# Kernel tuning notes

Measured on AMD Instinct MI355X. Metric: run time of the kernel, lower is better.

Reference implementation:

```python
import jax, jax.numpy as jnp
import numpy as np

NS = (50000, 12500, 3125, 800, 200)   # mesh vertex counts per hierarchy level
CS = (3, 16, 32, 64, 128)             # in_channels + out_channels per level
S = 9       # spiral length
K = 4       # nnz per row of pooling transforms
LATENT = 128
B = 32


def setup_inputs() -> dict:
    key = jax.random.key(0)
    ks = iter(jax.random.split(key, 80))
    inp = {"x": jax.random.normal(next(ks), (B, NS[0], 3), jnp.float32)}
    for l in range(4):
        inp["spiral%d" % l] = jax.random.randint(next(ks), (NS[l], S), 0, NS[l], dtype=jnp.int32)
        # down_transform[l]: sparse (NS[l+1], NS[l])
        inp["down_rows%d" % l] = jnp.repeat(jnp.arange(NS[l + 1], dtype=jnp.int32), K)
        inp["down_cols%d" % l] = jax.random.randint(next(ks), (NS[l + 1] * K,), 0, NS[l], dtype=jnp.int32)
        inp["down_vals%d" % l] = jnp.full((NS[l + 1] * K,), 1.0 / K, jnp.float32)
        # up_transform[l]: sparse (NS[l], NS[l+1])
        inp["up_rows%d" % l] = jnp.repeat(jnp.arange(NS[l], dtype=jnp.int32), K)
        inp["up_cols%d" % l] = jax.random.randint(next(ks), (NS[l] * K,), 0, NS[l + 1], dtype=jnp.int32)
        inp["up_vals%d" % l] = jnp.full((NS[l] * K,), 1.0 / K, jnp.float32)
        # encoder SpiralConv weights: Linear(C_in*S -> C_out), stored (in, out)
        inp["enW%d" % l] = jax.random.normal(next(ks), (CS[l] * S, CS[l + 1]), jnp.float32) * 0.05
        inp["enb%d" % l] = jnp.zeros((CS[l + 1],), jnp.float32)
    inp["muW"] = jax.random.normal(next(ks), (NS[4] * CS[4], LATENT), jnp.float32) * 0.02
    inp["mub"] = jnp.zeros((LATENT,), jnp.float32)
    inp["deW0"] = jax.random.normal(next(ks), (LATENT, NS[4] * CS[4]), jnp.float32) * 0.02
    inp["deb0"] = jnp.zeros((NS[4] * CS[4],), jnp.float32)
    dcin = (CS[4], CS[4], CS[3], CS[2])
    dcout = (CS[4], CS[3], CS[2], CS[1])
    for i in range(4):
        inp["dW%d" % i] = jax.random.normal(next(ks), (dcin[i] * S, dcout[i]), jnp.float32) * 0.05
        inp["db%d" % i] = jnp.zeros((dcout[i],), jnp.float32)
    inp["outW"] = jax.random.normal(next(ks), (CS[1] * S, 3), jnp.float32) * 0.05
    inp["outb"] = jnp.zeros((3,), jnp.float32)
    return inp


def _sconv(x, idx, W, b):
    # x: (B, N, C); idx: (N, S) -> gather spiral neighbors, flatten, dense Linear
    g = x[:, idx.reshape(-1), :].reshape(x.shape[0], idx.shape[0], -1)  # (B, N, S*C)
    return g @ W + b


def _pool(x, rows, cols, vals, M):
    # sparse (M, N) transform applied along vertex dim: index_select + scale + scatter_add
    out = jnp.zeros((x.shape[0], M, x.shape[2]), x.dtype)
    return out.at[:, rows].add(x[:, cols] * vals[None, :, None])


def _forward(x, spirals, downs, ups, enWs, enbs, muW, mub, deW0, deb0, dWs, dbs, outW, outb):
    # encode: (SpiralConv -> ELU -> Pool) x4
    h = x
    for l in range(4):
        h = jax.nn.elu(_sconv(h, spirals[l], enWs[l], enbs[l]))
        h = _pool(h, downs[l][0], downs[l][1], downs[l][2], NS[l + 1])
    h = h.reshape(h.shape[0], -1)  # (B, num_vert * C_last)
    mu = jax.nn.sigmoid(h @ muW + mub)  # is_vae=False path: sigmoid(mu), logvar=None
    z = mu
    # decode: Linear -> (Pool -> SpiralConv -> ELU) x4 -> SpiralConv
    d = (z @ deW0 + deb0).reshape(-1, NS[4], CS[4])
    for i in range(4):
        l = 3 - i
        d = _pool(d, ups[l][0], ups[l][1], ups[l][2], NS[l])
        d = jax.nn.elu(_sconv(d, spirals[l], dWs[i], dbs[i]))
    out = _sconv(d, spirals[0], outW, outb)
    return out, z, mu


def reference(x, spiral0, down_rows0, down_cols0, down_vals0, up_rows0, up_cols0, up_vals0, enW0, enb0, spiral1, down_rows1, down_cols1, down_vals1, up_rows1, up_cols1, up_vals1, enW1, enb1, spiral2, down_rows2, down_cols2, down_vals2, up_rows2, up_cols2, up_vals2, enW2, enb2, spiral3, down_rows3, down_cols3, down_vals3, up_rows3, up_cols3, up_vals3, enW3, enb3, muW, mub, deW0, deb0, dW0, db0, dW1, db1, dW2, db2, dW3, db3, outW, outb):
    spirals = [spiral0, spiral1, spiral2, spiral3]
    downs = [(down_rows0, down_cols0, down_vals0), (down_rows1, down_cols1, down_vals1), (down_rows2, down_cols2, down_vals2), (down_rows3, down_cols3, down_vals3)]
    ups = [(up_rows0, up_cols0, up_vals0), (up_rows1, up_cols1, up_vals1), (up_rows2, up_cols2, up_vals2), (up_rows3, up_cols3, up_vals3)]
    return _forward(x, spirals, downs, ups, [enW0, enW1, enW2, enW3], [enb0, enb1, enb2, enb3], muW, mub, deW0, deb0, [dW0, dW1, dW2, dW3], [db0, db1, db2, db3], outW, outb)
```

## Files before the change

### kernel.cpp

```cpp
#include <hip/hip_runtime.h>
#include <hip/hip_bf16.h>
#include <math.h>

#define NS0 50000
#define NS1 12500
#define NS2 3125
#define NS3 800
#define NS4 200
#define BATCH 32
#define SLEN 9

typedef __hip_bfloat16 bf16;
typedef __attribute__((ext_vector_type(8))) short short8_t;
typedef __attribute__((ext_vector_type(4))) float f32x4;

struct WcvAll {
    const float* W[9];
    bf16* dst[9];
    int K[9], CO[9], KP[9];
    int off[10];
};

__global__ void __launch_bounds__(256)
wconv_all_kernel(WcvAll p)
{
    int gid = blockIdx.x * 256 + threadIdx.x;
    if (gid >= p.off[9]) return;
    int seg = 0;
    #pragma unroll
    for (int s = 1; s < 9; ++s) seg += (gid >= p.off[s]);
    int local = gid - p.off[seg];
    int NKK = p.KP[seg] >> 5;
    int jj   = local & 7;
    int g8   = local >> 3;
    int lane = g8 & 63;
    int blk  = g8 >> 6;
    int kk   = blk % NKK;
    int cb   = blk / NKK;
    int col0 = lane & 15, kh = lane >> 4;
    int co = cb * 16 + col0;
    int k  = kk * 32 + kh * 8 + jj;
    float v = (k < p.K[seg] && co < p.CO[seg]) ? p.W[seg][k * p.CO[seg] + co] : 0.f;
    p.dst[seg][local] = __float2bfloat16(v);
}

__global__ void __launch_bounds__(256)
xpose_in_kernel(const float* __restrict__ x, bf16* __restrict__ xT)
{
    int tid = blockIdx.x * 256 + threadIdx.x;
    if (tid >= BATCH * NS0) return;
    int b = tid / NS0, n = tid - b * NS0;
    const float* src = x + (size_t)tid * 3;
    bf16* dst = xT + ((size_t)n * 32 + b) * 3;
    dst[0] = __float2bfloat16(src[0]);
    dst[1] = __float2bfloat16(src[1]);
    dst[2] = __float2bfloat16(src[2]);
}

__global__ void __launch_bounds__(256)
xpose_out_kernel(const float* __restrict__ vm, float* __restrict__ out)
{
    int tid = blockIdx.x * 256 + threadIdx.x;
    if (tid >= BATCH * NS0) return;
    int b = tid / NS0, n = tid - b * NS0;
    const float* src = vm + ((size_t)n * 32 + b) * 3;
    float* dst = out + (size_t)tid * 3;
    dst[0] = src[0];
    dst[1] = src[1];
    dst[2] = src[2];
}

__global__ void __launch_bounds__(256)
sconv_enc0(const bf16* __restrict__ xT, const int* __restrict__ idx,
           const bf16* __restrict__ Wfrag, const float* __restrict__ bias,
           bf16* __restrict__ y)
{
    __shared__ short lds[64 * 40];
    const int t = threadIdx.x;
    const int n0 = blockIdx.x * 2;

    for (int e = t; e < 64 * 5; e += 256) {
        int r = e / 5, k = 27 + (e - r * 5);
        lds[r * 40 + k] = 0;
    }
    for (int e = t; e < 2 * 9 * 32; e += 256) {
        int v = e / 288;
        int rem = e - v * 288;
        int s = rem >> 5, b = rem & 31;
        int j = idx[(n0 + v) * 9 + s];
        const short* src = (const short*)(xT + (size_t)j * 96 + b * 3);
        short* dst = &lds[(v * 32 + b) * 40 + s * 3];
        dst[0] = src[0];
        dst[1] = src[1];
        dst[2] = src[2];
    }
    __syncthreads();

    const int w = t >> 6, lane = t & 63;
    const int col0 = lane & 15, kh = lane >> 4;
    const int rbase = w * 16;
    float bv = bias[col0];
    f32x4 acc = (f32x4){bv, bv, bv, bv};
    short8_t bfr = *(const short8_t*)(Wfrag + (size_t)lane * 8);
    short8_t afr = *(const short8_t*)&lds[(rbase + col0) * 40 + kh * 8];
    acc = __builtin_amdgcn_mfma_f32_16x16x32_bf16(afr, bfr, acc, 0, 0, 0);
    #pragma unroll
    for (int i = 0; i < 4; ++i) {
        int rl = rbase + kh * 4 + i;
        float v = acc[i];
        v = v > 0.f ? v : expm1f(v);
        y[((size_t)n0 * 32 + rl) * 16 + col0] = __float2bfloat16(v);
    }
}

template<int CIN, int COUT, int COP, int ACT, int NN, typename TOUT>
__global__ void __launch_bounds__(256)
sconv_vm(const bf16* __restrict__ x, const int* __restrict__ idx,
         const bf16* __restrict__ Wfrag, const float* __restrict__ bias,
         TOUT* __restrict__ y)
{
    constexpr int KP  = (9 * CIN + 31) / 32 * 32;
    constexpr int NKK = KP / 32;
    constexpr int NCB = COP / 16;

    const int t = threadIdx.x, w = t >> 6, lane = t & 63;
    const int n = blockIdx.x * 4 + w;
    if (n >= NN) return;
    const int col0 = lane & 15, kh = lane >> 4;

    int jn[9];
    #pragma unroll
    for (int s = 0; s < 9; ++s) jn[s] = idx[n * 9 + s];

    f32x4 acc[2][NCB];
    #pragma unroll
    for (int cb = 0; cb < NCB; ++cb) {
        int col = cb * 16 + col0;
        float bv = (col < COUT) ? bias[col] : 0.f;
        acc[0][cb] = (f32x4){bv, bv, bv, bv};
        acc[1][cb] = (f32x4){bv, bv, bv, bv};
    }

    const short8_t z8 = {0, 0, 0, 0, 0, 0, 0, 0};
    #pragma unroll
    for (int kk = 0; kk < NKK; ++kk) {
        short8_t a0 = z8, a1 = z8;
        if constexpr (CIN == 16) {
            const int hi = kh >> 1;
            const int ch = (kh & 1) * 8;
            if (kk < 4) {
                int j = hi ? jn[2 * kk + 1] : jn[2 * kk];
                const bf16* base = x + (size_t)j * 512 + ch;
                a0 = *(const short8_t*)(base + col0 * 16);
                a1 = *(const short8_t*)(base + 256 + col0 * 16);
            } else {
                if (!hi) {
                    int j = jn[8];
                    const bf16* base = x + (size_t)j * 512 + ch;
                    a0 = *(const short8_t*)(base + col0 * 16);
                    a1 = *(const short8_t*)(base + 256 + col0 * 16);
                }
            }
        } else {
            constexpr int SPK = CIN / 32;
            const int j = jn[kk / SPK];
            const int ch = (kk % SPK) * 32 + kh * 8;
            const bf16* base = x + (size_t)j * (32 * CIN) + ch;
            a0 = *(const short8_t*)(base + col0 * CIN);
            a1 = *(const short8_t*)(base + (16 + col0) * CIN);
        }
        #pragma unroll
        for (int cb = 0; cb < NCB; ++cb) {
            short8_t bfr = *(const short8_t*)(Wfrag + ((size_t)(cb * NKK + kk) * 64 + lane) * 8);
            acc[0][cb] = __builtin_amdgcn_mfma_f32_16x16x32_bf16(a0, bfr, acc[0][cb], 0, 0, 0);
            acc[1][cb] = __builtin_amdgcn_mfma_f32_16x16x32_bf16(a1, bfr, acc[1][cb], 0, 0, 0);
        }
    }

    #pragma unroll
    for (int f = 0; f < 2; ++f) {
        #pragma unroll
        for (int cb = 0; cb < NCB; ++cb) {
            int col = cb * 16 + col0;
            if (col < COUT) {
                #pragma unroll
                for (int i = 0; i < 4; ++i) {
                    int b = f * 16 + kh * 4 + i;
                    float v = acc[f][cb][i];
                    if (ACT) v = v > 0.f ? v : expm1f(v);
                    TOUT* dst = &y[((size_t)n * 32 + b) * COUT + col];
                    if constexpr (__is_same(TOUT, float)) *dst = v;
                    else *dst = __float2bfloat16(v);
                }
            }
        }
    }
}

template<int C8>
__global__ void __launch_bounds__(256)
pool_vm(const bf16* __restrict__ x, const int* __restrict__ cols,
        const float* __restrict__ vals, bf16* __restrict__ y, int M)
{
    constexpr int BC8 = 32 * C8;
    int tid = blockIdx.x * 256 + threadIdx.x;
    if (tid >= M * BC8) return;
    int m = tid / BC8;
    int e = tid - m * BC8;
    const uint4* xv = (const uint4*)x;
    float acc[8];
    #pragma unroll
    for (int q = 0; q < 8; ++q) acc[q] = 0.f;
    #pragma unroll
    for (int j = 0; j < 4; ++j) {
        int col = cols[m * 4 + j];
        float v = vals[m * 4 + j];
        uint4 u = xv[(size_t)col * BC8 + e];
        const bf16* hh = (const bf16*)&u;
        #pragma unroll
        for (int q = 0; q < 8; ++q)
            acc[q] = fmaf(v, __bfloat162float(hh[q]), acc[q]);
    }
    uint4 o;
    bf16* oh = (bf16*)&o;
    #pragma unroll
    for (int q = 0; q < 8; ++q) oh[q] = __float2bfloat16(acc[q]);
    ((uint4*)y)[(size_t)m * BC8 + e] = o;
}

__global__ void __launch_bounds__(256)
mu_partial_kernel(const bf16* __restrict__ h, const float* __restrict__ W,
                  float* __restrict__ partial)
{
    __shared__ float hs[4096];
    const int t = threadIdx.x;
    const int nb = blockIdx.x;
    const bf16* hb = h + (size_t)nb * 4096;
    for (int e = t; e < 512; e += 256) {
        short8_t v = *(const short8_t*)(hb + e * 8);
        #pragma unroll
        for (int q = 0; q < 8; ++q)
            hs[e * 8 + q] = __bfloat162float(((const bf16*)&v)[q]);
    }
    __syncthreads();
    const int co = t & 127;
    const int bh = t >> 7;
    float acc[16];
    #pragma unroll
    for (int i = 0; i < 16; ++i) acc[i] = 0.f;
    const int k0 = nb * 128;
    for (int k = 0; k < 128; ++k) {
        float wv = W[(size_t)(k0 + k) * 128 + co];
        #pragma unroll
        for (int i = 0; i < 16; ++i)
            acc[i] = fmaf(hs[(bh * 16 + i) * 128 + k], wv, acc[i]);
    }
    float* pb = partial + (size_t)nb * 4096;
    #pragma unroll
    for (int i = 0; i < 16; ++i)
        pb[(bh * 16 + i) * 128 + co] = acc[i];
}

__global__ void __launch_bounds__(256)
mu_reduce_kernel(const float* __restrict__ partial, const float* __restrict__ bias,
                 float* __restrict__ z, float* __restrict__ out_z,
                 float* __restrict__ out_mu)
{
    const int i = blockIdx.x * 256 + threadIdx.x;
    const int co = i & 127;
    float a0 = 0.f, a1 = 0.f, a2 = 0.f, a3 = 0.f;
    #pragma unroll 4
    for (int c = 0; c < 200; c += 4) {
        a0 += partial[(size_t)c * 4096 + i];
        a1 += partial[(size_t)(c + 1) * 4096 + i];
        a2 += partial[(size_t)(c + 2) * 4096 + i];
        a3 += partial[(size_t)(c + 3) * 4096 + i];
    }
    float acc = (a0 + a1) + (a2 + a3) + bias[co];
    float m = 1.f / (1.f + expf(-acc));
    z[i] = m;
    out_z[i] = m;
    out_mu[i] = m;
}

__global__ void __launch_bounds__(256)
de0_kernel(const float* __restrict__ z, const float* __restrict__ W,
           const float* __restrict__ bias, bf16* __restrict__ d)
{
    __shared__ float zs[BATCH * 128];
    const int t = threadIdx.x;
    for (int e = t; e < BATCH * 128; e += 256) zs[e] = z[e];
    __syncthreads();
    const int j = blockIdx.x * 256 + t;
    float bj = bias[j];
    float acc[BATCH];
    #pragma unroll
    for (int b = 0; b < BATCH; ++b) acc[b] = bj;
    for (int k = 0; k < 128; ++k) {
        float w = W[k * 25600 + j];
        #pragma unroll
        for (int b = 0; b < BATCH; ++b)
            acc[b] = fmaf(zs[b * 128 + k], w, acc[b]);
    }
    const int nn = j >> 7, c = j & 127;
    #pragma unroll
    for (int b = 0; b < BATCH; ++b)
        d[(size_t)nn * 4096 + b * 128 + c] = __float2bfloat16(acc[b]);
}

extern "C" void kernel_launch(void* const* d_in, const int* in_sizes, int n_in,
                              void* d_out, int out_size, void* d_ws, size_t ws_size,
                              hipStream_t stream)
{
    const float* x = (const float*)d_in[0];
    const int*   sp[4];
    const int*   dn_cols[4];
    const float* dn_vals[4];
    const int*   up_cols[4];
    const float* up_vals[4];
    const float* enW[4];
    const float* enb[4];
    for (int l = 0; l < 4; ++l) {
        int base = 1 + 9 * l;
        sp[l]      = (const int*)d_in[base + 0];
        dn_cols[l] = (const int*)d_in[base + 2];
        dn_vals[l] = (const float*)d_in[base + 3];
        up_cols[l] = (const int*)d_in[base + 5];
        up_vals[l] = (const float*)d_in[base + 6];
        enW[l]     = (const float*)d_in[base + 7];
        enb[l]     = (const float*)d_in[base + 8];
    }
    const float* muW  = (const float*)d_in[37];
    const float* mub  = (const float*)d_in[38];
    const float* deW0 = (const float*)d_in[39];
    const float* deb0 = (const float*)d_in[40];
    const float* dW[4]  = { (const float*)d_in[41], (const float*)d_in[43],
                            (const float*)d_in[45], (const float*)d_in[47] };
    const float* db[4]  = { (const float*)d_in[42], (const float*)d_in[44],
                            (const float*)d_in[46], (const float*)d_in[48] };
    const float* outW = (const float*)d_in[49];
    const float* outb = (const float*)d_in[50];

    char* ws = (char*)d_ws;
    bf16*  A  = (bf16*)ws;
    bf16*  Bb = (bf16*)(ws + 51200000);
    bf16*  xT = (bf16*)(ws + 51200000);
    float* outVM = (float*)(ws + 51200000);
    float* Z  = (float*)(ws + 153600000);
    bf16*  wEN0 = (bf16*)(ws + 153600000 + 16384);
    bf16*  wOUT = wEN0 + 512;

    float* outF   = (float*)d_out;
    float* out_z  = outF + 4800000;
    float* out_mu = outF + 4804096;

    bf16*  wsc  = (bf16*)d_out;
    bf16*  wEN1 = wsc;
    bf16*  wEN2 = wsc + 5120;
    bf16*  wEN3 = wsc + 23552;
    bf16*  wDW0 = wsc + 97280;
    bf16*  wDW1 = wsc + 244736;
    bf16*  wDW2 = wsc + 318464;
    bf16*  wDW3 = wsc + 336896;
    float* muPart = outF + 1000000;

    WcvAll wp;
    const float* srcs[9] = {enW[0], enW[1], enW[2], enW[3], dW[0], dW[1], dW[2], dW[3], outW};
    bf16* dsts[9] = {wEN0, wEN1, wEN2, wEN3, wDW0, wDW1, wDW2, wDW3, wOUT};
    int Ks[9]   = {27, 144, 288, 576, 1152, 1152, 576, 288, 144};
    int COs[9]  = {16, 32, 64, 128, 128, 64, 32, 16, 3};
    int KPs[9]  = {32, 160, 288, 576, 1152, 1152, 576, 288, 160};
    int COPs[9] = {16, 32, 64, 128, 128, 64, 32, 16, 16};
    int off = 0;
    for (int s = 0; s < 9; ++s) {
        wp.W[s] = srcs[s]; wp.dst[s] = dsts[s];
        wp.K[s] = Ks[s]; wp.CO[s] = COs[s]; wp.KP[s] = KPs[s];
        wp.off[s] = off; off += COPs[s] * KPs[s];
    }
    wp.off[9] = off;
    auto cdiv = [](int a, int b) { return (a + b - 1) / b; };
    wconv_all_kernel<<<cdiv(off, 256), 256, 0, stream>>>(wp);

    xpose_in_kernel<<<cdiv(BATCH * NS0, 256), 256, 0, stream>>>(x, xT);

    sconv_enc0<<<NS0 / 2, 256, 0, stream>>>(xT, sp[0], wEN0, enb[0], A);
    pool_vm<2><<<cdiv(NS1 * 64, 256), 256, 0, stream>>>(A, dn_cols[0], dn_vals[0], Bb, NS1);
    sconv_vm<16, 32, 32, 1, NS1, bf16><<<cdiv(NS1, 4), 256, 0, stream>>>(Bb, sp[1], wEN1, enb[1], A);
    pool_vm<4><<<cdiv(NS2 * 128, 256), 256, 0, stream>>>(A, dn_cols[1], dn_vals[1], Bb, NS2);
    sconv_vm<32, 64, 64, 1, NS2, bf16><<<cdiv(NS2, 4), 256, 0, stream>>>(Bb, sp[2], wEN2, enb[2], A);
    pool_vm<8><<<cdiv(NS3 * 256, 256), 256, 0, stream>>>(A, dn_cols[2], dn_vals[2], Bb, NS3);
    sconv_vm<64, 128, 128, 1, NS3, bf16><<<cdiv(NS3, 4), 256, 0, stream>>>(Bb, sp[3], wEN3, enb[3], A);
    pool_vm<16><<<cdiv(NS4 * 512, 256), 256, 0, stream>>>(A, dn_cols[3], dn_vals[3], Bb, NS4);

    mu_partial_kernel<<<200, 256, 0, stream>>>(Bb, muW, muPart);
    mu_reduce_kernel<<<16, 256, 0, stream>>>(muPart, mub, Z, out_z, out_mu);
    de0_kernel<<<25600 / 256, 256, 0, stream>>>(Z, deW0, deb0, A);

    pool_vm<16><<<cdiv(NS3 * 512, 256), 256, 0, stream>>>(A, up_cols[3], up_vals[3], Bb, NS3);
    sconv_vm<128, 128, 128, 1, NS3, bf16><<<cdiv(NS3, 4), 256, 0, stream>>>(Bb, sp[3], wDW0, db[0], A);
    pool_vm<16><<<cdiv(NS2 * 512, 256), 256, 0, stream>>>(A, up_cols[2], up_vals[2], Bb, NS2);
    sconv_vm<128, 64, 64, 1, NS2, bf16><<<cdiv(NS2, 4), 256, 0, stream>>>(Bb, sp[2], wDW1, db[1], A);
    pool_vm<8><<<cdiv(NS1 * 256, 256), 256, 0, stream>>>(A, up_cols[1], up_vals[1], Bb, NS1);
    sconv_vm<64, 32, 32, 1, NS1, bf16><<<cdiv(NS1, 4), 256, 0, stream>>>(Bb, sp[1], wDW2, db[2], A);
    pool_vm<4><<<cdiv(NS0 * 128, 256), 256, 0, stream>>>(A, up_cols[0], up_vals[0], Bb, NS0);
    sconv_vm<32, 16, 16, 1, NS0, bf16><<<cdiv(NS0, 4), 256, 0, stream>>>(Bb, sp[0], wDW3, db[3], A);

    sconv_vm<16, 3, 16, 0, NS0, float><<<cdiv(NS0, 4), 256, 0, stream>>>(A, sp[0], wOUT, outb, outVM);
    xpose_out_kernel<<<cdiv(BATCH * NS0, 256), 256, 0, stream>>>(outVM, outF);
}
```

Baseline: 821.3 us.

## Prefetch spiral gathers in chunks, tile transposes through LDS, add occupancy hints

The spiral conv kernel now issues all neighbor-feature gathers up front, or in double-buffered chunks of six k-steps for wide layers, before the MFMA loop, so that gather latency overlaps with matrix math. Launch bounds now request a minimum of 4 or 2 waves per SIMD depending on K depth. The input and output transposes stage an 8-vertex by 32-batch tile in LDS so that both the global reads and the global writes are contiguous. The risks are higher register pressure from the prefetch buffers and possible spilling under the occupancy hint.

```diff
diff --git a/kernel.cpp b/kernel.cpp
--- a/kernel.cpp
+++ b/kernel.cpp
@@ -47,27 +47,39 @@
 __global__ void __launch_bounds__(256)
 xpose_in_kernel(const float* __restrict__ x, bf16* __restrict__ xT)
 {
-    int tid = blockIdx.x * 256 + threadIdx.x;
-    if (tid >= BATCH * NS0) return;
-    int b = tid / NS0, n = tid - b * NS0;
-    const float* src = x + (size_t)tid * 3;
-    bf16* dst = xT + ((size_t)n * 32 + b) * 3;
-    dst[0] = __float2bfloat16(src[0]);
-    dst[1] = __float2bfloat16(src[1]);
-    dst[2] = __float2bfloat16(src[2]);
+    __shared__ short ldsb[256 * 3];
+    const int t = threadIdx.x;
+    const int n0 = blockIdx.x * 8;
+    const int b = t >> 3, v = t & 7;
+    const float* src = x + ((size_t)b * NS0 + n0 + v) * 3;
+    short* d = &ldsb[(v * 32 + b) * 3];
+    d[0] = __bfloat16_as_short(__float2bfloat16(src[0]));
+    d[1] = __bfloat16_as_short(__float2bfloat16(src[1]));
+    d[2] = __bfloat16_as_short(__float2bfloat16(src[2]));
+    __syncthreads();
+    short* dst = (short*)xT + ((size_t)n0 * 32 + t) * 3;
+    dst[0] = ldsb[t * 3 + 0];
+    dst[1] = ldsb[t * 3 + 1];
+    dst[2] = ldsb[t * 3 + 2];
 }
 
 __global__ void __launch_bounds__(256)
 xpose_out_kernel(const float* __restrict__ vm, float* __restrict__ out)
 {
-    int tid = blockIdx.x * 256 + threadIdx.x;
-    if (tid >= BATCH * NS0) return;
-    int b = tid / NS0, n = tid - b * NS0;
-    const float* src = vm + ((size_t)n * 32 + b) * 3;
-    float* dst = out + (size_t)tid * 3;
-    dst[0] = src[0];
-    dst[1] = src[1];
-    dst[2] = src[2];
+    __shared__ float ldsf[256 * 3];
+    const int t = threadIdx.x;
+    const int n0 = blockIdx.x * 8;
+    const float* src = vm + ((size_t)n0 * 32 + t) * 3;
+    ldsf[t * 3 + 0] = src[0];
+    ldsf[t * 3 + 1] = src[1];
+    ldsf[t * 3 + 2] = src[2];
+    __syncthreads();
+    const int b = t >> 3, v = t & 7;
+    float* dst = out + ((size_t)b * NS0 + n0 + v) * 3;
+    const float* s = &ldsf[(v * 32 + b) * 3];
+    dst[0] = s[0];
+    dst[1] = s[1];
+    dst[2] = s[2];
 }
 
 __global__ void __launch_bounds__(256)
@@ -114,7 +126,8 @@
 }
 
 template<int CIN, int COUT, int COP, int ACT, int NN, typename TOUT>
-__global__ void __launch_bounds__(256)
+__global__ void
+__launch_bounds__(256, (((9 * CIN + 31) / 32 * 32 / 32) <= 9) ? 4 : 2)
 sconv_vm(const bf16* __restrict__ x, const int* __restrict__ idx,
          const bf16* __restrict__ Wfrag, const float* __restrict__ bias,
          TOUT* __restrict__ y)
@@ -122,6 +135,9 @@
     constexpr int KP  = (9 * CIN + 31) / 32 * 32;
     constexpr int NKK = KP / 32;
     constexpr int NCB = COP / 16;
+    constexpr int CH  = (NKK <= 9) ? NKK : 6;
+    constexpr int NCHUNK = NKK / CH;
+    constexpr int NBUF = (NCHUNK > 1) ? 2 : 1;
 
     const int t = threadIdx.x, w = t >> 6, lane = t & 63;
     const int n = blockIdx.x * 4 + w;
@@ -142,9 +158,8 @@
     }
 
     const short8_t z8 = {0, 0, 0, 0, 0, 0, 0, 0};
-    #pragma unroll
-    for (int kk = 0; kk < NKK; ++kk) {
-        short8_t a0 = z8, a1 = z8;
+    auto loadA = [&](int kk, short8_t& a0, short8_t& a1) {
+        a0 = z8; a1 = z8;
         if constexpr (CIN == 16) {
             const int hi = kh >> 1;
             const int ch = (kh & 1) * 8;
@@ -153,13 +168,11 @@
                 const bf16* base = x + (size_t)j * 512 + ch;
                 a0 = *(const short8_t*)(base + col0 * 16);
                 a1 = *(const short8_t*)(base + 256 + col0 * 16);
-            } else {
-                if (!hi) {
-                    int j = jn[8];
-                    const bf16* base = x + (size_t)j * 512 + ch;
-                    a0 = *(const short8_t*)(base + col0 * 16);
-                    a1 = *(const short8_t*)(base + 256 + col0 * 16);
-                }
+            } else if (!hi) {
+                int j = jn[8];
+                const bf16* base = x + (size_t)j * 512 + ch;
+                a0 = *(const short8_t*)(base + col0 * 16);
+                a1 = *(const short8_t*)(base + 256 + col0 * 16);
             }
         } else {
             constexpr int SPK = CIN / 32;
@@ -169,11 +182,31 @@
             a0 = *(const short8_t*)(base + col0 * CIN);
             a1 = *(const short8_t*)(base + (16 + col0) * CIN);
         }
-        #pragma unroll
-        for (int cb = 0; cb < NCB; ++cb) {
-            short8_t bfr = *(const short8_t*)(Wfrag + ((size_t)(cb * NKK + kk) * 64 + lane) * 8);
-            acc[0][cb] = __builtin_amdgcn_mfma_f32_16x16x32_bf16(a0, bfr, acc[0][cb], 0, 0, 0);
-            acc[1][cb] = __builtin_amdgcn_mfma_f32_16x16x32_bf16(a1, bfr, acc[1][cb], 0, 0, 0);
+    };
+
+    short8_t bufA[NBUF][2 * CH];
+    #pragma unroll
+    for (int q = 0; q < CH; ++q)
+        loadA(q, bufA[0][2 * q], bufA[0][2 * q + 1]);
+
+    #pragma unroll
+    for (int c = 0; c < NCHUNK; ++c) {
+        const int cur = (NBUF > 1) ? (c & 1) : 0;
+        if (c + 1 < NCHUNK) {
+            const int nxt = (NBUF > 1) ? ((c + 1) & 1) : 0;
+            #pragma unroll
+            for (int q = 0; q < CH; ++q)
+                loadA((c + 1) * CH + q, bufA[nxt][2 * q], bufA[nxt][2 * q + 1]);
+        }
+        #pragma unroll
+        for (int q = 0; q < CH; ++q) {
+            const int kk = c * CH + q;
+            #pragma unroll
+            for (int cb = 0; cb < NCB; ++cb) {
+                short8_t bfr = *(const short8_t*)(Wfrag + ((size_t)(cb * NKK + kk) * 64 + lane) * 8);
+                acc[0][cb] = __builtin_amdgcn_mfma_f32_16x16x32_bf16(bufA[cur][2 * q],     bfr, acc[0][cb], 0, 0, 0);
+                acc[1][cb] = __builtin_amdgcn_mfma_f32_16x16x32_bf16(bufA[cur][2 * q + 1], bfr, acc[1][cb], 0, 0, 0);
+            }
         }
     }
 
@@ -381,7 +414,7 @@
     auto cdiv = [](int a, int b) { return (a + b - 1) / b; };
     wconv_all_kernel<<<cdiv(off, 256), 256, 0, stream>>>(wp);
 
-    xpose_in_kernel<<<cdiv(BATCH * NS0, 256), 256, 0, stream>>>(x, xT);
+    xpose_in_kernel<<<NS0 / 8, 256, 0, stream>>>(x, xT);
 
     sconv_enc0<<<NS0 / 2, 256, 0, stream>>>(xT, sp[0], wEN0, enb[0], A);
     pool_vm<2><<<cdiv(NS1 * 64, 256), 256, 0, stream>>>(A, dn_cols[0], dn_vals[0], Bb, NS1);
@@ -406,5 +439,5 @@
     sconv_vm<32, 16, 16, 1, NS0, bf16><<<cdiv(NS0, 4), 256, 0, stream>>>(Bb, sp[0], wDW3, db[3], A);
 
     sconv_vm<16, 3, 16, 0, NS0, float><<<cdiv(NS0, 4), 256, 0, stream>>>(A, sp[0], wOUT, outb, outVM);
-    xpose_out_kernel<<<cdiv(BATCH * NS0, 256), 256, 0, stream>>>(outVM, outF);
-}
+    xpose_out_kernel<<<NS0 / 8, 256, 0, stream>>>(outVM, outF);
+}
```

Result: faster. 756.7 us (-7.9%).
